# Performance work log

Hardware: AMD Instinct MI355X
Metric: run time of the kernel (lower is better)

Reference implementation:

```python
import jax, jax.numpy as jnp
import numpy as np
from jax import lax

B, C, H, W = 256, 6, 100, 128
LAT = 4
NEG = 0.01  # F.leaky_relu default slope


def lrelu(x):
    return jnp.where(x >= 0, x, NEG * x)


def conv(x, w, b):
    # submanifold 3x3 conv on fully-dense active set == SAME dense conv
    y = lax.conv_general_dilated(x, w, (1, 1), 'SAME',
                                 dimension_numbers=('NCHW', 'OIHW', 'NCHW'))
    return y + b[None, :, None, None]


def maxpool(x, kh, kw):
    return lax.reduce_window(x, -jnp.inf, lax.max,
                             (1, 1, kh, kw), (1, 1, kh, kw), 'VALID')


def invconv(x, w, b):
    # SparseInverseConv2d with stride == kernel (non-overlapping): exact
    # transposed conv restoring the pre-pool grid. w: (Cin, Cout, kh, kw)
    b_, c, h, wd = x.shape
    co, kh, kw = w.shape[1], w.shape[2], w.shape[3]
    y = jnp.einsum('bchw,cokl->bohkwl', x, w).reshape(b_, co, h * kh, wd * kw)
    return y + b[None, :, None, None]


def setup_inputs() -> dict:
    key = jax.random.key(0)
    ks = jax.random.split(key, 32)
    rn = lambda k, s, sc=0.05: jax.random.normal(k, s, jnp.float32) * sc
    return {
        'x':   jax.random.normal(ks[0], (B, C, H, W), jnp.float32),
        'eps': jax.random.normal(ks[1], (B * 2 * 16, LAT), jnp.float32),
        'w1': rn(ks[2], (8, 6, 3, 3)),   'b1': rn(ks[3], (8,), 0.01),
        'w2': rn(ks[4], (16, 8, 3, 3)),  'b2': rn(ks[5], (16,), 0.01),
        'w3': rn(ks[6], (32, 16, 3, 3)), 'b3': rn(ks[7], (32,), 0.01),
        'wmu': rn(ks[8], (32, LAT)),  'bmu': rn(ks[9], (LAT,), 0.01),
        'wlv': rn(ks[10], (32, LAT)), 'blv': rn(ks[11], (LAT,), 0.01),
        'wlin': rn(ks[12], (LAT, 32)), 'blin': rn(ks[13], (32,), 0.01),
        'wi1': rn(ks[14], (32, 32, 5, 2)), 'bi1': rn(ks[15], (32,), 0.01),
        'w4': rn(ks[16], (16, 32, 3, 3)),  'b4': rn(ks[17], (16,), 0.01),
        'wi2': rn(ks[18], (16, 16, 5, 2)), 'bi2': rn(ks[19], (16,), 0.01),
        'w5': rn(ks[20], (8, 16, 3, 3)),   'b5': rn(ks[21], (8,), 0.01),
        'wi3': rn(ks[22], (8, 8, 2, 2)),   'bi3': rn(ks[23], (8,), 0.01),
        'w6': rn(ks[24], (6, 8, 3, 3)),    'b6': rn(ks[25], (6,), 0.01),
    }


def reference(x, eps, w1, b1, w2, b2, w3, b3, wmu, bmu, wlv, blv, wlin, blin,
              wi1, bi1, w4, b4, wi2, bi2, w5, b5, wi3, bi3, w6, b6):
    # encoder
    p1 = maxpool(lrelu(conv(x, w1, b1)), 2, 2)    # (B,8,50,64)
    p2 = maxpool(lrelu(conv(p1, w2, b2)), 5, 2)   # (B,16,10,32)
    p3 = maxpool(lrelu(conv(p2, w3, b3)), 5, 2)   # (B,32,2,16)
    Bc, Cc, Hc, Wc = p3.shape
    feats = p3.transpose(0, 2, 3, 1).reshape(-1, Cc)  # (N=B*32, 32)
    mu = feats @ wmu + bmu
    logvar = feats @ wlv + blv
    z = mu + eps * jnp.exp(0.5 * logvar)
    # KL per cell, scatter_mean over batch index == per-event mean over cells
    kld_cell = -0.5 * jnp.sum(1.0 + logvar - mu * mu - jnp.exp(logvar), axis=-1)
    kld = kld_cell.reshape(Bc, Hc * Wc).mean(axis=-1)  # (B,)
    # decoder
    dec = (z @ wlin + blin).reshape(Bc, Hc, Wc, Cc).transpose(0, 3, 1, 2)
    u1 = lrelu(invconv(dec, wi1, bi1))            # (B,32,10,32)
    h4 = lrelu(conv(u1, w4, b4))
    u2 = lrelu(invconv(h4, wi2, bi2))             # (B,16,50,64)
    h5 = lrelu(conv(u2, w5, b5))
    u3 = lrelu(invconv(h5, wi3, bi3))             # (B,8,100,128)
    out = conv(u3, w6, b6)                        # (B,6,100,128)
    return out, mu, logvar, kld, z
```

## Files before the change

### kernel.cpp

```cpp
#include <hip/hip_runtime.h>
#include <hip/hip_bf16.h>

#define DEV __device__ __forceinline__

static DEV float lrelu(float v) { return v >= 0.f ? v : 0.01f * v; }
static DEV float bflo(unsigned u) { return __uint_as_float(u << 16); }
static DEV float bfhi(unsigned u) { return __uint_as_float(u & 0xffff0000u); }
static DEV unsigned short f2bf(float f) {
  unsigned u = __float_as_uint(f);
  return (unsigned short)((u + 0x7FFF + ((u >> 16) & 1)) >> 16);
}
static DEV unsigned pk(float a, float b) {
  return (unsigned)f2bf(a) | ((unsigned)f2bf(b) << 16);
}

constexpr int BATCH = 256;

constexpr size_t BYTE_B = 13107200;
constexpr size_t BYTE_C = 18350080;
constexpr size_t BYTE_D = 19398656;

__global__ __launch_bounds__(256, 1) void k1_conv1_pool(
    const float* __restrict__ x, const float* __restrict__ w1,
    const float* __restrict__ b1, __hip_bfloat16* __restrict__ p1) {
  __shared__ float4 xs[2640];
  __shared__ unsigned wcl[288];
  __shared__ float bsh[8];
  const int b = blockIdx.x, yt = blockIdx.y, tid = threadIdx.x;
  for (int i = tid; i < 288; i += 256) {
    const int cp = i & 3, co = (i >> 2) & 7, k = i >> 5;
    const int c0 = cp * 2;
    const float wa = (c0 < 6) ? w1[(co * 6 + c0) * 9 + k] : 0.f;
    const float wb = (c0 + 1 < 6) ? w1[(co * 6 + c0 + 1) * 9 + k] : 0.f;
    wcl[i] = pk(wa, wb);
  }
  if (tid < 8) bsh[tid] = b1[tid];
  for (int p = tid; p < 1300; p += 256) {
    const int lx = p % 130, ly = p / 130;
    const int gy = 8 * yt - 1 + ly, gx = lx - 1;
    float v[6];
    if ((unsigned)gy < 100u && (unsigned)gx < 128u) {
      #pragma unroll
      for (int c = 0; c < 6; ++c) v[c] = x[((size_t)(b * 6 + c) * 100 + gy) * 128 + gx];
    } else {
      #pragma unroll
      for (int c = 0; c < 6; ++c) v[c] = 0.f;
    }
    const int base = ly * 4224;
    const int sw = (((lx >> 2) & 7) << 4) ^ ((ly & 1) << 4);
    *(float4*)((char*)xs + base + ((lx * 32) ^ sw)) = make_float4(v[0], v[1], v[2], v[3]);
    *(float2*)((char*)xs + base + ((lx * 32 + 16) ^ sw)) = make_float2(v[4], v[5]);
  }
  __syncthreads();
  {
    const int ox = tid & 63, oyy = tid >> 6;
    const int oyg = 4 * yt + oyy;
    float in[4][4][6];
    #pragma unroll
    for (int ry = 0; ry < 4; ++ry)
      #pragma unroll
      for (int cx = 0; cx < 4; ++cx) {
        const int lr = 2 * oyy + ry, lc = 2 * ox + cx;
        const int base = lr * 4224;
        const int sw = (((lc >> 2) & 7) << 4) ^ ((lr & 1) << 4);
        const float4 lo = *(const float4*)((const char*)xs + base + ((lc * 32) ^ sw));
        const float2 hi = *(const float2*)((const char*)xs + base + ((lc * 32 + 16) ^ sw));
        in[ry][cx][0] = lo.x; in[ry][cx][1] = lo.y; in[ry][cx][2] = lo.z;
        in[ry][cx][3] = lo.w; in[ry][cx][4] = hi.x; in[ry][cx][5] = hi.y;
      }
    float ev[8][2][2];
    #pragma unroll
    for (int co = 0; co < 8; ++co) {
      const float bv = bsh[co];
      ev[co][0][0] = bv; ev[co][0][1] = bv; ev[co][1][0] = bv; ev[co][1][1] = bv;
    }
    #pragma unroll
    for (int k = 0; k < 9; ++k) {
      const int ky = k / 3, kx = k % 3;
      #pragma unroll
      for (int co = 0; co < 8; ++co) {
        const uint4 wq = *(const uint4*)&wcl[(k * 8 + co) * 4];
        const float w0 = bflo(wq.x), w1v = bfhi(wq.x);
        const float w2v = bflo(wq.y), w3v = bfhi(wq.y);
        const float w4v = bflo(wq.z), w5v = bfhi(wq.z);
        #pragma unroll
        for (int dy = 0; dy < 2; ++dy)
          #pragma unroll
          for (int dx = 0; dx < 2; ++dx) {
            const float* ip = in[dy + ky][dx + kx];
            float a = ev[co][dy][dx];
            a += ip[0] * w0;  a += ip[1] * w1v; a += ip[2] * w2v;
            a += ip[3] * w3v; a += ip[4] * w4v; a += ip[5] * w5v;
            ev[co][dy][dx] = a;
          }
      }
    }
    if (oyg < 50) {
      #pragma unroll
      for (int co = 0; co < 8; ++co) {
        const float m = fmaxf(fmaxf(lrelu(ev[co][0][0]), lrelu(ev[co][0][1])),
                              fmaxf(lrelu(ev[co][1][0]), lrelu(ev[co][1][1])));
        p1[((size_t)(b * 8 + co) * 50 + oyg) * 64 + ox] = __float2bfloat16(m);
      }
    }
  }
}

__global__ __launch_bounds__(256, 1) void k2_conv2_pool(
    const __hip_bfloat16* __restrict__ p1, const float* __restrict__ w2,
    const float* __restrict__ b2, float* __restrict__ p2) {
  __shared__ float4 s1[1904];
  __shared__ float wsh[1152];
  __shared__ float bsh[16];
  const int b = blockIdx.x, yt = blockIdx.y, tid = threadIdx.x;
  for (int i = tid; i < 1152; i += 256) {
    const int ci = i & 7, co = (i >> 3) & 15, k = i >> 7;
    wsh[i] = w2[(co * 8 + ci) * 9 + k];
  }
  if (tid < 16) bsh[tid] = b2[tid];
  for (int p = tid; p < 462; p += 256) {
    const int lx = p % 66, ly = p / 66;
    const int gy = 5 * yt - 1 + ly, gx = lx - 1;
    float v[8];
    if ((unsigned)gy < 50u && (unsigned)gx < 64u) {
      #pragma unroll
      for (int c = 0; c < 8; ++c)
        v[c] = __bfloat162float(p1[((size_t)(b * 8 + c) * 50 + gy) * 64 + gx]);
    } else {
      #pragma unroll
      for (int c = 0; c < 8; ++c) v[c] = 0.f;
    }
    const int base = ly * 4352;
    const int sw = (((lx >> 2) & 7) << 4) ^ ((ly & 1) << 4);
    *(float4*)((char*)s1 + base + ((lx * 32) ^ sw)) = make_float4(v[0], v[1], v[2], v[3]);
    *(float4*)((char*)s1 + base + ((lx * 32 + 16) ^ sw)) = make_float4(v[4], v[5], v[6], v[7]);
  }
  __syncthreads();
  {
    const int ox = tid & 31, cog = tid >> 5;
    const int co0 = cog * 2;
    float ev[2][5][2];
    #pragma unroll
    for (int j = 0; j < 2; ++j) {
      const float bv = bsh[co0 + j];
      #pragma unroll
      for (int dy = 0; dy < 5; ++dy) { ev[j][dy][0] = bv; ev[j][dy][1] = bv; }
    }
    #pragma unroll
    for (int k = 0; k < 9; ++k) {
      const int ky = k / 3, kx = k % 3;
      float wr[2][8];
      #pragma unroll
      for (int j = 0; j < 2; ++j) {
        const float4 lo = *(const float4*)&wsh[(k * 16 + co0 + j) * 8];
        const float4 hi = *(const float4*)&wsh[(k * 16 + co0 + j) * 8 + 4];
        wr[j][0] = lo.x; wr[j][1] = lo.y; wr[j][2] = lo.z; wr[j][3] = lo.w;
        wr[j][4] = hi.x; wr[j][5] = hi.y; wr[j][6] = hi.z; wr[j][7] = hi.w;
      }
      #pragma unroll
      for (int dy = 0; dy < 5; ++dy) {
        const int lr = dy + ky;
        const int base = lr * 4352;
        const int rsw = (lr & 1) << 4;
        float in2[2][8];
        #pragma unroll
        for (int dx = 0; dx < 2; ++dx) {
          const int lc = 2 * ox + dx + kx;
          const int sw = (((lc >> 2) & 7) << 4) ^ rsw;
          const float4 lo = *(const float4*)((const char*)s1 + base + ((lc * 32) ^ sw));
          const float4 hi = *(const float4*)((const char*)s1 + base + ((lc * 32 + 16) ^ sw));
          in2[dx][0] = lo.x; in2[dx][1] = lo.y; in2[dx][2] = lo.z; in2[dx][3] = lo.w;
          in2[dx][4] = hi.x; in2[dx][5] = hi.y; in2[dx][6] = hi.z; in2[dx][7] = hi.w;
        }
        #pragma unroll
        for (int j = 0; j < 2; ++j)
          #pragma unroll
          for (int dx = 0; dx < 2; ++dx)
            #pragma unroll
            for (int ci = 0; ci < 8; ++ci)
              ev[j][dy][dx] += in2[dx][ci] * wr[j][ci];
      }
    }
    #pragma unroll
    for (int j = 0; j < 2; ++j) {
      float m = -1e30f;
      #pragma unroll
      for (int dy = 0; dy < 5; ++dy)
        #pragma unroll
        for (int dx = 0; dx < 2; ++dx)
          m = fmaxf(m, lrelu(ev[j][dy][dx]));
      p2[((size_t)(b * 16 + co0 + j) * 10 + yt) * 32 + ox] = m;
    }
  }
}

__global__ __launch_bounds__(256) void k3_conv3_pool(
    const float* __restrict__ p2, const float* __restrict__ w3,
    const float* __restrict__ b3, float* __restrict__ p3) {
  __shared__ float s2[16][12][34];
  __shared__ float wsh[4608];
  __shared__ float bsh[32];
  const int b = blockIdx.x, tid = threadIdx.x;
  for (int i = tid; i < 4608; i += 256) wsh[i] = w3[i];
  if (tid < 32) bsh[tid] = b3[tid];
  for (int i = tid; i < 16 * 12 * 34; i += 256) {
    int col = i % 34, rem = i / 34, r = rem % 12, c = rem / 12;
    int gy = r - 1, gx = col - 1;
    float v = 0.f;
    if ((unsigned)gy < 10u && (unsigned)gx < 32u)
      v = p2[((b * 16 + c) * 10 + gy) * 32 + gx];
    s2[c][r][col] = v;
  }
  __syncthreads();
  for (int i = tid; i < 1024; i += 256) {
    int ow = i & 15, rem = i >> 4, oh = rem & 1, co = rem >> 1;
    float m = -1e30f;
    for (int dy = 0; dy < 5; ++dy)
      #pragma unroll
      for (int dx = 0; dx < 2; ++dx) {
        int cy = 5 * oh + dy, cx = 2 * ow + dx;
        float acc = bsh[co];
        #pragma unroll
        for (int ci = 0; ci < 16; ++ci)
          #pragma unroll
          for (int ky = 0; ky < 3; ++ky)
            #pragma unroll
            for (int kx = 0; kx < 3; ++kx)
              acc += s2[ci][cy + ky][cx + kx] * wsh[(co * 16 + ci) * 9 + ky * 3 + kx];
        m = fmaxf(m, lrelu(acc));
      }
    p3[((b * 32 + co) * 2 + oh) * 16 + ow] = m;
  }
}

__global__ __launch_bounds__(64) void k4_latent(
    const float* __restrict__ p3, const float* __restrict__ eps,
    const float* __restrict__ wmu, const float* __restrict__ bmu,
    const float* __restrict__ wlv, const float* __restrict__ blv,
    const float* __restrict__ wlin, const float* __restrict__ blin,
    float* __restrict__ dec, float* __restrict__ out,
    size_t off_mu, size_t off_lv, size_t off_kld, size_t off_z) {
  const int b = blockIdx.x, t = threadIdx.x;
  __shared__ float skld[32];
  if (t < 32) {
    const int h = t >> 4, w = t & 15;
    float f[32];
    #pragma unroll
    for (int c = 0; c < 32; ++c) f[c] = p3[((b * 32 + c) * 2 + h) * 16 + w];
    const int n = b * 32 + t;
    float mu[4], lv[4], zz[4];
    #pragma unroll
    for (int j = 0; j < 4; ++j) {
      float m = bmu[j], l = blv[j];
      #pragma unroll
      for (int c = 0; c < 32; ++c) { m += f[c] * wmu[c * 4 + j]; l += f[c] * wlv[c * 4 + j]; }
      mu[j] = m; lv[j] = l;
      zz[j] = m + eps[n * 4 + j] * expf(0.5f * l);
    }
    float kc = 0.f;
    #pragma unroll
    for (int j = 0; j < 4; ++j) kc += 1.f + lv[j] - mu[j] * mu[j] - expf(lv[j]);
    skld[t] = -0.5f * kc;
    #pragma unroll
    for (int j = 0; j < 4; ++j) {
      out[off_mu + n * 4 + j] = mu[j];
      out[off_lv + n * 4 + j] = lv[j];
      out[off_z  + n * 4 + j] = zz[j];
    }
    for (int co = 0; co < 32; ++co) {
      float d = blin[co];
      #pragma unroll
      for (int j = 0; j < 4; ++j) d += zz[j] * wlin[j * 32 + co];
      dec[((b * 32 + co) * 2 + h) * 16 + w] = d;
    }
  }
  __syncthreads();
  if (t == 0) {
    float s = 0.f;
    for (int i = 0; i < 32; ++i) s += skld[i];
    out[off_kld + b] = s * (1.f / 32.f);
  }
}

__global__ __launch_bounds__(256) void k5_inv1_conv4(
    const float* __restrict__ dec, const float* __restrict__ wi1,
    const float* __restrict__ bi1, const float* __restrict__ w4,
    const float* __restrict__ b4, float* __restrict__ h4) {
  __shared__ float sdec[1024];
  __shared__ float su1[32][12][34];
  const int b = blockIdx.x, tid = threadIdx.x;
  for (int i = tid; i < 1024; i += 256) sdec[i] = dec[b * 1024 + i];
  for (int i = tid; i < 32 * 12 * 34; i += 256) ((float*)su1)[i] = 0.f;
  __syncthreads();
  for (int i = tid; i < 32 * 10 * 32; i += 256) {
    int X = i & 31, rem = i >> 5, Y = rem % 10, c = rem / 10;
    int hh = Y / 5, ky = Y % 5, wp = X >> 1, kx = X & 1;
    float acc = bi1[c];
    #pragma unroll
    for (int ci = 0; ci < 32; ++ci)
      acc += sdec[(ci * 2 + hh) * 16 + wp] * wi1[((ci * 32 + c) * 5 + ky) * 2 + kx];
    su1[c][Y + 1][X + 1] = lrelu(acc);
  }
  __syncthreads();
  for (int i = tid; i < 16 * 10 * 32; i += 256) {
    int X = i & 31, rem = i >> 5, Y = rem % 10, o = rem / 10;
    float acc = b4[o];
    for (int c = 0; c < 32; ++c)
      #pragma unroll
      for (int ky = 0; ky < 3; ++ky)
        #pragma unroll
        for (int kx = 0; kx < 3; ++kx)
          acc += su1[c][Y + ky][X + kx] * w4[((o * 32 + c) * 3 + ky) * 3 + kx];
    h4[((b * 16 + o) * 10 + Y) * 32 + X] = lrelu(acc);
  }
}

__global__ __launch_bounds__(256, 1) void k6_inv2_conv5(
    const float* __restrict__ h4, const float* __restrict__ wi2,
    const float* __restrict__ bi2, const float* __restrict__ w5,
    const float* __restrict__ b5, __hip_bfloat16* __restrict__ h5) {
  __shared__ uint4 su[1584];
  __shared__ float sh4cl[4][32][16];
  __shared__ unsigned wcl[1280];
  __shared__ float w5sh[1152];
  const int b = blockIdx.x, yt = blockIdx.y, tid = threadIdx.x;
  const int y0 = 10 * yt;
  const int r0 = (y0 == 0) ? 0 : (y0 - 1) / 5;
  for (int i = tid; i < 2048; i += 256) {
    const int ci = i & 15, hc = (i >> 4) & 31, r = i >> 9;
    const int gr = r0 + r;
    sh4cl[r][hc][ci] = (gr < 10) ? h4[((b * 16 + ci) * 10 + gr) * 32 + hc] : 0.f;
  }
  for (int i = tid; i < 1280; i += 256) {
    const int cp = i & 7, ci = (i >> 3) & 15, tap = i >> 7;
    const int ky = tap >> 1, kx = tap & 1;
    const int c0 = cp * 2;
    const float wa = wi2[((ci * 16 + c0) * 5 + ky) * 2 + kx];
    const float wb = wi2[((ci * 16 + c0 + 1) * 5 + ky) * 2 + kx];
    wcl[i] = pk(wa, wb);
  }
  for (int i = tid; i < 1152; i += 256) {
    const int ci = i & 15, o = (i >> 4) & 7, k = i >> 7;
    w5sh[i] = w5[((o * 16 + ci) * 3 + (k / 3)) * 3 + (k % 3)];
  }
  __syncthreads();
  for (int pos = tid; pos < 792; pos += 256) {
    const int lx = pos % 66, ly = pos / 66;
    const int Y = y0 - 1 + ly, X = lx - 1;
    float u[16];
    if ((unsigned)Y < 50u && (unsigned)X < 64u) {
      const int hr = Y / 5 - r0, ky = Y % 5, hc = X >> 1, kx = X & 1;
      const int tap = ky * 2 + kx;
      #pragma unroll
      for (int c = 0; c < 16; ++c) u[c] = bi2[c];
      float hv[16];
      #pragma unroll
      for (int q = 0; q < 4; ++q) {
        const float4 t = *(const float4*)&sh4cl[hr][hc][q * 4];
        hv[q * 4 + 0] = t.x; hv[q * 4 + 1] = t.y; hv[q * 4 + 2] = t.z; hv[q * 4 + 3] = t.w;
      }
      #pragma unroll
      for (int ci = 0; ci < 16; ++ci) {
        const uint4 wq0 = *(const uint4*)&wcl[(tap * 16 + ci) * 8];
        const uint4 wq1 = *(const uint4*)&wcl[(tap * 16 + ci) * 8 + 4];
        const float h = hv[ci];
        u[0]  += h * bflo(wq0.x); u[1]  += h * bfhi(wq0.x);
        u[2]  += h * bflo(wq0.y); u[3]  += h * bfhi(wq0.y);
        u[4]  += h * bflo(wq0.z); u[5]  += h * bfhi(wq0.z);
        u[6]  += h * bflo(wq0.w); u[7]  += h * bfhi(wq0.w);
        u[8]  += h * bflo(wq1.x); u[9]  += h * bfhi(wq1.x);
        u[10] += h * bflo(wq1.y); u[11] += h * bfhi(wq1.y);
        u[12] += h * bflo(wq1.z); u[13] += h * bfhi(wq1.z);
        u[14] += h * bflo(wq1.w); u[15] += h * bfhi(wq1.w);
      }
      #pragma unroll
      for (int c = 0; c < 16; ++c) u[c] = lrelu(u[c]);
    } else {
      #pragma unroll
      for (int c = 0; c < 16; ++c) u[c] = 0.f;
    }
    const int sw = (((lx >> 2) & 7) << 4) ^ ((ly & 1) << 4);
    *(uint4*)((char*)su + ly * 2112 + ((lx * 32) ^ sw)) =
        make_uint4(pk(u[0], u[1]), pk(u[2], u[3]), pk(u[4], u[5]), pk(u[6], u[7]));
    *(uint4*)((char*)su + ly * 2112 + ((lx * 32 + 16) ^ sw)) =
        make_uint4(pk(u[8], u[9]), pk(u[10], u[11]), pk(u[12], u[13]), pk(u[14], u[15]));
  }
  __syncthreads();
  {
    const int x = tid & 63, yg = tid >> 6;
    float acc[3][8];
    #pragma unroll
    for (int r = 0; r < 3; ++r)
      #pragma unroll
      for (int o = 0; o < 8; ++o) acc[r][o] = b5[o];
    #pragma unroll
    for (int k = 0; k < 9; ++k) {
      const int ky = k / 3, kx = k % 3;
      const int p = x + kx;
      const int csw = ((p >> 2) & 7) << 4;
      #pragma unroll
      for (int half = 0; half < 2; ++half) {
        float wr[4][16];
        #pragma unroll
        for (int o2 = 0; o2 < 4; ++o2) {
          const int o = half * 4 + o2;
          #pragma unroll
          for (int q = 0; q < 4; ++q) {
            const float4 t = *(const float4*)&w5sh[(k * 8 + o) * 16 + q * 4];
            wr[o2][q * 4 + 0] = t.x; wr[o2][q * 4 + 1] = t.y;
            wr[o2][q * 4 + 2] = t.z; wr[o2][q * 4 + 3] = t.w;
          }
        }
        #pragma unroll
        for (int r = 0; r < 3; ++r) {
          const int rr = yg + 4 * r;
          if (rr < 10) {
            const int ly = rr + ky;
            const int rowb = ly * 2112;
            const int sw = csw ^ ((ly & 1) << 4);
            const uint4 q0 = *(const uint4*)((const char*)su + rowb + ((p * 32) ^ sw));
            const uint4 q1 = *(const uint4*)((const char*)su + rowb + ((p * 32 + 16) ^ sw));
            float v[16];
            v[0]  = bflo(q0.x); v[1]  = bfhi(q0.x); v[2]  = bflo(q0.y); v[3]  = bfhi(q0.y);
            v[4]  = bflo(q0.z); v[5]  = bfhi(q0.z); v[6]  = bflo(q0.w); v[7]  = bfhi(q0.w);
            v[8]  = bflo(q1.x); v[9]  = bfhi(q1.x); v[10] = bflo(q1.y); v[11] = bfhi(q1.y);
            v[12] = bflo(q1.z); v[13] = bfhi(q1.z); v[14] = bflo(q1.w); v[15] = bfhi(q1.w);
            #pragma unroll
            for (int o2 = 0; o2 < 4; ++o2) {
              float a = acc[r][half * 4 + o2];
              #pragma unroll
              for (int c = 0; c < 16; ++c)
                a += v[c] * wr[o2][c];
              acc[r][half * 4 + o2] = a;
            }
          }
        }
      }
    }
    #pragma unroll
    for (int r = 0; r < 3; ++r) {
      const int rr = yg + 4 * r;
      if (rr < 10) {
        const int Y = y0 + rr;
        uint4 w = make_uint4(pk(lrelu(acc[r][0]), lrelu(acc[r][1])),
                             pk(lrelu(acc[r][2]), lrelu(acc[r][3])),
                             pk(lrelu(acc[r][4]), lrelu(acc[r][5])),
                             pk(lrelu(acc[r][6]), lrelu(acc[r][7])));
        *(uint4*)&h5[(((size_t)b * 50 + Y) * 64 + x) * 8] = w;
      }
    }
  }
}

__global__ __launch_bounds__(256, 1) void k7_inv3_conv6(
    const __hip_bfloat16* __restrict__ h5, const float* __restrict__ wi3,
    const float* __restrict__ bi3, const float* __restrict__ w6,
    const float* __restrict__ b6, float* __restrict__ out) {
  __shared__ float4 su[3168];
  __shared__ float wsh[432];
  __shared__ float bsh[6];
  const int b = blockIdx.x, yt = blockIdx.y, tid = threadIdx.x;
  const int y0 = 10 * yt;
  for (int i = tid; i < 432; i += 256) {
    const int ci = i & 7, rem = i >> 3, o = rem % 6, k = rem / 6;
    wsh[i] = w6[((o * 8 + ci) * 3 + (k / 3)) * 3 + (k % 3)];
  }
  if (tid < 6) bsh[tid] = b6[tid];
  {
    const int lyp = (tid >> 1) & 1, lxp = tid & 1;
    const int ky = (lyp + 1) & 1, kx = (lxp + 1) & 1;
    float wr[8][8];
    #pragma unroll
    for (int ci = 0; ci < 8; ++ci)
      #pragma unroll
      for (int c = 0; c < 8; ++c)
        wr[ci][c] = wi3[((ci * 8 + c) * 2 + ky) * 2 + kx];
    float bs[8];
    #pragma unroll
    for (int c = 0; c < 8; ++c) bs[c] = bi3[c];
    for (int p = tid >> 2; p < 390; p += 64) {
      const int ly = lyp + 2 * (p / 65);
      const int lx = lxp + 2 * (p % 65);
      const int yy = y0 - 1 + ly, xx2 = lx - 1;
      float u[8];
      if ((unsigned)yy < 100u && (unsigned)xx2 < 128u) {
        const uint4 hv = *(const uint4*)&h5[(((size_t)b * 50 + (yy >> 1)) * 64 + (xx2 >> 1)) * 8];
        const float v0 = bflo(hv.x), v1 = bfhi(hv.x), v2 = bflo(hv.y), v3 = bfhi(hv.y);
        const float v4 = bflo(hv.z), v5 = bfhi(hv.z), v6 = bflo(hv.w), v7 = bfhi(hv.w);
        #pragma unroll
        for (int c = 0; c < 8; ++c) {
          float a = bs[c];
          a += v0 * wr[0][c]; a += v1 * wr[1][c]; a += v2 * wr[2][c]; a += v3 * wr[3][c];
          a += v4 * wr[4][c]; a += v5 * wr[5][c]; a += v6 * wr[6][c]; a += v7 * wr[7][c];
          u[c] = lrelu(a);
        }
      } else {
        #pragma unroll
        for (int c = 0; c < 8; ++c) u[c] = 0.f;
      }
      const int base = ly * 4224;
      const int sw = (((lx >> 2) & 7) << 4) ^ ((ly & 1) << 4);
      *(float4*)((char*)su + base + ((lx * 32) ^ sw)) = make_float4(u[0], u[1], u[2], u[3]);
      *(float4*)((char*)su + base + ((lx * 32 + 16) ^ sw)) = make_float4(u[4], u[5], u[6], u[7]);
    }
  }
  __syncthreads();
  {
    const int x = tid & 127, yb = tid >> 7;
    float acc[5][6];
    #pragma unroll
    for (int r = 0; r < 5; ++r)
      #pragma unroll
      for (int o = 0; o < 6; ++o) acc[r][o] = bsh[o];
    #pragma unroll
    for (int k = 0; k < 9; ++k) {
      const int ky = k / 3, kx = k % 3;
      float wr[6][8];
      #pragma unroll
      for (int o = 0; o < 6; ++o) {
        const float4 wlo = *(const float4*)&wsh[(k * 6 + o) * 8];
        const float4 whi = *(const float4*)&wsh[(k * 6 + o) * 8 + 4];
        wr[o][0] = wlo.x; wr[o][1] = wlo.y; wr[o][2] = wlo.z; wr[o][3] = wlo.w;
        wr[o][4] = whi.x; wr[o][5] = whi.y; wr[o][6] = whi.z; wr[o][7] = whi.w;
      }
      const int lc = x + kx;
      const int csw = ((lc >> 2) & 7) << 4;
      #pragma unroll
      for (int r = 0; r < 5; ++r) {
        const int lr = yb + 2 * r + ky;
        const int base = lr * 4224;
        const int sw = csw ^ ((lr & 1) << 4);
        const float4 lo = *(const float4*)((const char*)su + base + ((lc * 32) ^ sw));
        const float4 hi = *(const float4*)((const char*)su + base + ((lc * 32 + 16) ^ sw));
        const float v[8] = {lo.x, lo.y, lo.z, lo.w, hi.x, hi.y, hi.z, hi.w};
        #pragma unroll
        for (int o = 0; o < 6; ++o)
          #pragma unroll
          for (int ci = 0; ci < 8; ++ci)
            acc[r][o] += v[ci] * wr[o][ci];
      }
    }
    #pragma unroll
    for (int r = 0; r < 5; ++r) {
      const int Y = y0 + yb + 2 * r;
      #pragma unroll
      for (int o = 0; o < 6; ++o)
        out[((size_t)(b * 6 + o) * 100 + Y) * 128 + x] = acc[r][o];
    }
  }
}

extern "C" void kernel_launch(void* const* d_in, const int* in_sizes, int n_in,
                              void* d_out, int out_size, void* d_ws, size_t ws_size,
                              hipStream_t stream) {
  const float* x    = (const float*)d_in[0];
  const float* eps  = (const float*)d_in[1];
  const float* w1   = (const float*)d_in[2];
  const float* b1   = (const float*)d_in[3];
  const float* w2   = (const float*)d_in[4];
  const float* b2   = (const float*)d_in[5];
  const float* w3   = (const float*)d_in[6];
  const float* b3   = (const float*)d_in[7];
  const float* wmu  = (const float*)d_in[8];
  const float* bmu  = (const float*)d_in[9];
  const float* wlv  = (const float*)d_in[10];
  const float* blv  = (const float*)d_in[11];
  const float* wlin = (const float*)d_in[12];
  const float* blin = (const float*)d_in[13];
  const float* wi1  = (const float*)d_in[14];
  const float* bi1  = (const float*)d_in[15];
  const float* w4   = (const float*)d_in[16];
  const float* b4   = (const float*)d_in[17];
  const float* wi2  = (const float*)d_in[18];
  const float* bi2  = (const float*)d_in[19];
  const float* w5   = (const float*)d_in[20];
  const float* b5   = (const float*)d_in[21];
  const float* wi3  = (const float*)d_in[22];
  const float* bi3  = (const float*)d_in[23];
  const float* w6   = (const float*)d_in[24];
  const float* b6   = (const float*)d_in[25];

  char* wsb = (char*)d_ws;
  __hip_bfloat16* p1 = (__hip_bfloat16*)wsb;
  __hip_bfloat16* h5 = (__hip_bfloat16*)wsb;
  float* p2  = (float*)(wsb + BYTE_B);
  float* h4  = (float*)(wsb + BYTE_B);
  float* p3  = (float*)(wsb + BYTE_C);
  float* dec = (float*)(wsb + BYTE_D);
  float* out = (float*)d_out;

  const size_t off_z   = (size_t)out_size - 32768;
  const size_t off_kld = off_z - 256;
  const size_t off_lv  = off_kld - 32768;
  const size_t off_mu  = off_lv - 32768;

  k1_conv1_pool<<<dim3(BATCH, 13), 256, 0, stream>>>(x, w1, b1, p1);
  k2_conv2_pool<<<dim3(BATCH, 10), 256, 0, stream>>>(p1, w2, b2, p2);
  k3_conv3_pool<<<dim3(BATCH), 256, 0, stream>>>(p2, w3, b3, p3);
  k4_latent<<<dim3(BATCH), 64, 0, stream>>>(p3, eps, wmu, bmu, wlv, blv, wlin, blin,
                                            dec, out, off_mu, off_lv, off_kld, off_z);
  k5_inv1_conv4<<<dim3(BATCH), 256, 0, stream>>>(dec, wi1, bi1, w4, b4, h4);
  k6_inv2_conv5<<<dim3(BATCH, 5), 256, 0, stream>>>(h4, wi2, bi2, w5, b5, h5);
  k7_inv3_conv6<<<dim3(BATCH, 10), 256, 0, stream>>>(h5, wi3, bi3, w6, b6, out);
}
```

Measured before the change: 587.8 us.

## Restructure conv1+pool to one pooled row per block with bf16 LDS tile

The first conv+maxpool kernel now has each block compute one pooled output row, with each thread producing one conv pixel. Pooling goes through a shared-memory reduction instead of each thread holding a 4x4x6 input patch and computing a 2x2 window in registers. The input tile is stored in LDS as packed bf16 (uint4 per pixel), which cuts LDS footprint and raises the grid from 13 to 50 row tiles per image. This lowers register pressure and improves parallelism. In exchange it adds halo reloads (4 rows per 2 output rows), an extra barrier, a pooling phase where only 64 of 256 threads work, and bf16 rounding of the input.

```diff
diff --git a/kernel.cpp b/kernel.cpp
--- a/kernel.cpp
+++ b/kernel.cpp
@@ -23,7 +23,8 @@
 __global__ __launch_bounds__(256, 1) void k1_conv1_pool(
     const float* __restrict__ x, const float* __restrict__ w1,
     const float* __restrict__ b1, __hip_bfloat16* __restrict__ p1) {
-  __shared__ float4 xs[2640];
+  __shared__ uint4 xs[4 * 132];
+  __shared__ float4 pc[512];
   __shared__ unsigned wcl[288];
   __shared__ float bsh[8];
   const int b = blockIdx.x, yt = blockIdx.y, tid = threadIdx.x;
@@ -35,9 +36,9 @@
     wcl[i] = pk(wa, wb);
   }
   if (tid < 8) bsh[tid] = b1[tid];
-  for (int p = tid; p < 1300; p += 256) {
+  for (int p = tid; p < 520; p += 256) {
     const int lx = p % 130, ly = p / 130;
-    const int gy = 8 * yt - 1 + ly, gx = lx - 1;
+    const int gy = 2 * yt - 1 + ly, gx = lx - 1;
     float v[6];
     if ((unsigned)gy < 100u && (unsigned)gx < 128u) {
       #pragma unroll
@@ -46,63 +47,54 @@
       #pragma unroll
       for (int c = 0; c < 6; ++c) v[c] = 0.f;
     }
-    const int base = ly * 4224;
-    const int sw = (((lx >> 2) & 7) << 4) ^ ((ly & 1) << 4);
-    *(float4*)((char*)xs + base + ((lx * 32) ^ sw)) = make_float4(v[0], v[1], v[2], v[3]);
-    *(float2*)((char*)xs + base + ((lx * 32 + 16) ^ sw)) = make_float2(v[4], v[5]);
+    xs[ly * 132 + lx] = make_uint4(pk(v[0], v[1]), pk(v[2], v[3]), pk(v[4], v[5]), 0u);
   }
   __syncthreads();
   {
-    const int ox = tid & 63, oyy = tid >> 6;
-    const int oyg = 4 * yt + oyy;
-    float in[4][4][6];
-    #pragma unroll
-    for (int ry = 0; ry < 4; ++ry)
-      #pragma unroll
-      for (int cx = 0; cx < 4; ++cx) {
-        const int lr = 2 * oyy + ry, lc = 2 * ox + cx;
-        const int base = lr * 4224;
-        const int sw = (((lc >> 2) & 7) << 4) ^ ((lr & 1) << 4);
-        const float4 lo = *(const float4*)((const char*)xs + base + ((lc * 32) ^ sw));
-        const float2 hi = *(const float2*)((const char*)xs + base + ((lc * 32 + 16) ^ sw));
-        in[ry][cx][0] = lo.x; in[ry][cx][1] = lo.y; in[ry][cx][2] = lo.z;
-        in[ry][cx][3] = lo.w; in[ry][cx][4] = hi.x; in[ry][cx][5] = hi.y;
-      }
-    float ev[8][2][2];
-    #pragma unroll
-    for (int co = 0; co < 8; ++co) {
-      const float bv = bsh[co];
-      ev[co][0][0] = bv; ev[co][0][1] = bv; ev[co][1][0] = bv; ev[co][1][1] = bv;
-    }
+    const int cy = tid >> 7, cx = tid & 127;
+    float ev[8];
+    #pragma unroll
+    for (int co = 0; co < 8; ++co) ev[co] = bsh[co];
     #pragma unroll
     for (int k = 0; k < 9; ++k) {
       const int ky = k / 3, kx = k % 3;
+      const uint4 q = xs[(cy + ky) * 132 + (cx + kx)];
+      const float i0 = bflo(q.x), i1 = bfhi(q.x);
+      const float i2 = bflo(q.y), i3 = bfhi(q.y);
+      const float i4 = bflo(q.z), i5 = bfhi(q.z);
       #pragma unroll
       for (int co = 0; co < 8; ++co) {
         const uint4 wq = *(const uint4*)&wcl[(k * 8 + co) * 4];
-        const float w0 = bflo(wq.x), w1v = bfhi(wq.x);
-        const float w2v = bflo(wq.y), w3v = bfhi(wq.y);
-        const float w4v = bflo(wq.z), w5v = bfhi(wq.z);
-        #pragma unroll
-        for (int dy = 0; dy < 2; ++dy)
-          #pragma unroll
-          for (int dx = 0; dx < 2; ++dx) {
-            const float* ip = in[dy + ky][dx + kx];
-            float a = ev[co][dy][dx];
-            a += ip[0] * w0;  a += ip[1] * w1v; a += ip[2] * w2v;
-            a += ip[3] * w3v; a += ip[4] * w4v; a += ip[5] * w5v;
-            ev[co][dy][dx] = a;
-          }
-      }
-    }
-    if (oyg < 50) {
-      #pragma unroll
-      for (int co = 0; co < 8; ++co) {
-        const float m = fmaxf(fmaxf(lrelu(ev[co][0][0]), lrelu(ev[co][0][1])),
-                              fmaxf(lrelu(ev[co][1][0]), lrelu(ev[co][1][1])));
-        p1[((size_t)(b * 8 + co) * 50 + oyg) * 64 + ox] = __float2bfloat16(m);
-      }
-    }
+        float a = ev[co];
+        a += i0 * bflo(wq.x); a += i1 * bfhi(wq.x);
+        a += i2 * bflo(wq.y); a += i3 * bfhi(wq.y);
+        a += i4 * bflo(wq.z); a += i5 * bfhi(wq.z);
+        ev[co] = a;
+      }
+    }
+    float4* pp = &pc[(cy * 128 + cx) * 2];
+    pp[0] = make_float4(lrelu(ev[0]), lrelu(ev[1]), lrelu(ev[2]), lrelu(ev[3]));
+    pp[1] = make_float4(lrelu(ev[4]), lrelu(ev[5]), lrelu(ev[6]), lrelu(ev[7]));
+  }
+  __syncthreads();
+  if (tid < 64) {
+    const int ox = tid;
+    const float4 a0 = pc[(2 * ox) * 2],       a1 = pc[(2 * ox) * 2 + 1];
+    const float4 b0 = pc[(2 * ox + 1) * 2],   b1 = pc[(2 * ox + 1) * 2 + 1];
+    const float4 c0 = pc[(128 + 2 * ox) * 2], c1 = pc[(128 + 2 * ox) * 2 + 1];
+    const float4 d0 = pc[(128 + 2 * ox + 1) * 2], d1 = pc[(128 + 2 * ox + 1) * 2 + 1];
+    float m[8];
+    m[0] = fmaxf(fmaxf(a0.x, b0.x), fmaxf(c0.x, d0.x));
+    m[1] = fmaxf(fmaxf(a0.y, b0.y), fmaxf(c0.y, d0.y));
+    m[2] = fmaxf(fmaxf(a0.z, b0.z), fmaxf(c0.z, d0.z));
+    m[3] = fmaxf(fmaxf(a0.w, b0.w), fmaxf(c0.w, d0.w));
+    m[4] = fmaxf(fmaxf(a1.x, b1.x), fmaxf(c1.x, d1.x));
+    m[5] = fmaxf(fmaxf(a1.y, b1.y), fmaxf(c1.y, d1.y));
+    m[6] = fmaxf(fmaxf(a1.z, b1.z), fmaxf(c1.z, d1.z));
+    m[7] = fmaxf(fmaxf(a1.w, b1.w), fmaxf(c1.w, d1.w));
+    #pragma unroll
+    for (int co = 0; co < 8; ++co)
+      p1[((size_t)(b * 8 + co) * 50 + yt) * 64 + ox] = __float2bfloat16(m[co]);
   }
 }
 
@@ -594,7 +586,7 @@
   const size_t off_lv  = off_kld - 32768;
   const size_t off_mu  = off_lv - 32768;
 
-  k1_conv1_pool<<<dim3(BATCH, 13), 256, 0, stream>>>(x, w1, b1, p1);
+  k1_conv1_pool<<<dim3(BATCH, 50), 256, 0, stream>>>(x, w1, b1, p1);
   k2_conv2_pool<<<dim3(BATCH, 10), 256, 0, stream>>>(p1, w2, b2, p2);
   k3_conv3_pool<<<dim3(BATCH), 256, 0, stream>>>(p2, w3, b3, p3);
   k4_latent<<<dim3(BATCH), 64, 0, stream>>>(p3, eps, wmu, bmu, wlv, blv, wlin, blin,
```

Measured after the change: 546.9 us. 6.9% less time.
